# Kernel tuning notes

Hardware: AMD Instinct MI355X
Metric: run time of the kernel (lower is better)

Reference implementation:

```python
import jax, jax.numpy as jnp
import numpy as np
from jax import lax

B, C, H, W = 256, 7, 128, 128   # batch, num_bands, img_size, img_size
HID = 256                        # scorer hidden width
SEL = 3                          # selected_bands


def setup_inputs() -> dict:
    key = jax.random.key(0)
    k = jax.random.split(key, 7)
    n = H * W
    x = jax.random.normal(k[0], (B, C, H, W), dtype=jnp.float32)
    # to_qkv: Linear(num_bands, 3*num_bands); stored (in, out) for x @ w. Dead code
    # in the original forward (attn_output unused) but kept for parameter parity.
    w_qkv = jax.random.normal(k[1], (C, 3 * C), dtype=jnp.float32) * (1.0 / np.sqrt(C))
    b_qkv = jnp.zeros((3 * C,), dtype=jnp.float32)
    # band_score_proj: Linear(n, 256) -> ReLU -> Linear(256, 1)
    w1 = jax.random.normal(k[2], (n, HID), dtype=jnp.float32) * (1.0 / np.sqrt(n))
    b1 = jax.random.normal(k[3], (HID,), dtype=jnp.float32) * 0.01
    w2 = jax.random.normal(k[4], (HID, 1), dtype=jnp.float32) * (1.0 / np.sqrt(HID))
    b2 = jax.random.normal(k[5], (1,), dtype=jnp.float32) * 0.01
    return {"x": x, "w_qkv": w_qkv, "b_qkv": b_qkv, "w1": w1, "b1": b1, "w2": w2, "b2": b2}


def reference(x, w_qkv, b_qkv, w1, b1, w2, b2):
    b, c, h, w = x.shape
    feat = x.reshape(b, c, h * w)                  # b c n  (== x_flat.transpose(1,2))
    # NOTE: the original also runs a 1-dim-per-head SDPA on x_flat whose result
    # (attn_output) is never used in the returned values; it is omitted here.
    hid = jax.nn.relu(jnp.einsum('bcn,nk->bck', feat, w1) + b1)   # b c 256
    band_scores = (jnp.einsum('bck,ko->bco', hid, w2) + b2)[..., 0]  # b c
    _, top_indices = lax.top_k(band_scores, SEL)                  # b sel
    selected = jnp.take_along_axis(x, top_indices[:, :, None, None], axis=1)  # b sel h w
    return selected, top_indices
```

## Files before the change

### kernel.cpp

```cpp
#include <hip/hip_runtime.h>

#define Bn    256
#define Cc    7
#define Nn    16384
#define HIDW  256
#define SEL   3
#define Mrows (Bn * Cc)
#define KSPLIT 16
#define KCHUNK (Nn / KSPLIT)
#define BK    32
#define PART_STRIDE ((size_t)Mrows * HIDW)

typedef __attribute__((ext_vector_type(8))) short bf16x8;
typedef __attribute__((ext_vector_type(4))) float floatx4;

#if __has_builtin(__builtin_amdgcn_global_load_lds)
#define HAS_GLDS 1
#endif

#if __has_builtin(__builtin_amdgcn_sched_barrier)
#define SCHED_FENCE() __builtin_amdgcn_sched_barrier(0)
#else
#define SCHED_FENCE()
#endif

__device__ __forceinline__ unsigned pack_hi16(unsigned ua, unsigned ub) {
#if __has_builtin(__builtin_amdgcn_perm)
    return __builtin_amdgcn_perm(ub, ua, 0x07060302u);
#else
    return (ua >> 16) | (ub & 0xffff0000u);
#endif
}

__device__ __forceinline__ void split2(float a, float b, unsigned& hp, unsigned& lp) {
    unsigned ua = __float_as_uint(a), ub = __float_as_uint(b);
    float fa = __uint_as_float(ua & 0xffff0000u);
    float fb = __uint_as_float(ub & 0xffff0000u);
    float la = a - fa, lb = b - fb;
    hp = pack_hi16(ua, ub);
    lp = pack_hi16(__float_as_uint(la), __float_as_uint(lb));
}

__global__ __launch_bounds__(256) void convert_w1(const float* __restrict__ w1,
                                                  unsigned short* __restrict__ bhi,
                                                  unsigned short* __restrict__ blo) {
    const int id = blockIdx.x * 256 + threadIdx.x;
    const int l  = id & 63;
    const int ct = id >> 6;
    const int T  = ct & 15;
    const int c  = ct >> 4;
    const int n  = T * 16 + (l & 15);
    const int k  = c * 32 + (l >> 4) * 8;
    float f[8];
#pragma unroll
    for (int j = 0; j < 8; ++j) f[j] = w1[(size_t)(k + j) * HIDW + n];
    unsigned hp[4], lp[4];
#pragma unroll
    for (int m = 0; m < 4; ++m) split2(f[2 * m], f[2 * m + 1], hp[m], lp[m]);
    *(uint4*)(bhi + (size_t)id * 8) = make_uint4(hp[0], hp[1], hp[2], hp[3]);
    *(uint4*)(blo + (size_t)id * 8) = make_uint4(lp[0], lp[1], lp[2], lp[3]);
}

__global__ __launch_bounds__(256) void gemm_mfma(const float* __restrict__ A,
                                                 const unsigned short* __restrict__ Bhi,
                                                 const unsigned short* __restrict__ Blo,
                                                 float* __restrict__ part) {
    __shared__ unsigned short Ah[4096], Al[4096], Bh[4096], Bl[4096];

    const int bx = blockIdx.x;
    const int m0 = blockIdx.y * 128;
    const int s  = blockIdx.z;
    const int k0 = s * KCHUNK;
    const int t  = threadIdx.x;
    const int lane = t & 63;
    const int w    = t >> 6;
    const int wm   = w & 1;
    const int wn   = w >> 1;

    const int ar  = t >> 1;
    const int kof = (t & 1) * 16;
    const float* aptr = A + (size_t)(m0 + ar) * Nn + k0 + kof;
    const int aidx0 = (ar >> 4) * 512 + ((ar & 15) + ((kof >> 3) + 0) * 16) * 8;
    const int aidx1 = (ar >> 4) * 512 + ((ar & 15) + ((kof >> 3) + 1) * 16) * 8;
    const int wbase = (t & 192) * 8;

    floatx4 acc[4][4];
#pragma unroll
    for (int i = 0; i < 4; ++i)
#pragma unroll
        for (int j = 0; j < 4; ++j) acc[i][j] = (floatx4)0.0f;

    float4 pa0 = *(const float4*)(aptr + 0);
    float4 pa1 = *(const float4*)(aptr + 4);
    float4 pa2 = *(const float4*)(aptr + 8);
    float4 pa3 = *(const float4*)(aptr + 12);

    for (int kk = 0; kk < KCHUNK; kk += BK) {
        float af[16] = {pa0.x, pa0.y, pa0.z, pa0.w, pa1.x, pa1.y, pa1.z, pa1.w,
                        pa2.x, pa2.y, pa2.z, pa2.w, pa3.x, pa3.y, pa3.z, pa3.w};
        unsigned hp[8], lp[8];
#pragma unroll
        for (int m = 0; m < 8; ++m) split2(af[2 * m], af[2 * m + 1], hp[m], lp[m]);

        SCHED_FENCE();
        __builtin_amdgcn_s_barrier();
        SCHED_FENCE();

        const size_t bbase = ((size_t)(((k0 + kk) >> 5) * 16 + bx * 8)) * 512;
#ifdef HAS_GLDS
        __builtin_amdgcn_global_load_lds(
            (const __attribute__((address_space(1))) void*)(Bhi + bbase + t * 8),
            (__attribute__((address_space(3))) void*)&Bh[wbase], 16, 0, 0);
        __builtin_amdgcn_global_load_lds(
            (const __attribute__((address_space(1))) void*)(Bhi + bbase + 2048 + t * 8),
            (__attribute__((address_space(3))) void*)&Bh[2048 + wbase], 16, 0, 0);
        __builtin_amdgcn_global_load_lds(
            (const __attribute__((address_space(1))) void*)(Blo + bbase + t * 8),
            (__attribute__((address_space(3))) void*)&Bl[wbase], 16, 0, 0);
        __builtin_amdgcn_global_load_lds(
            (const __attribute__((address_space(1))) void*)(Blo + bbase + 2048 + t * 8),
            (__attribute__((address_space(3))) void*)&Bl[2048 + wbase], 16, 0, 0);
#else
        *(uint4*)&Bh[t * 8]        = *(const uint4*)(Bhi + bbase + t * 8);
        *(uint4*)&Bh[2048 + t * 8] = *(const uint4*)(Bhi + bbase + 2048 + t * 8);
        *(uint4*)&Bl[t * 8]        = *(const uint4*)(Blo + bbase + t * 8);
        *(uint4*)&Bl[2048 + t * 8] = *(const uint4*)(Blo + bbase + 2048 + t * 8);
#endif
        SCHED_FENCE();

        *(uint4*)&Ah[aidx0] = make_uint4(hp[0], hp[1], hp[2], hp[3]);
        *(uint4*)&Ah[aidx1] = make_uint4(hp[4], hp[5], hp[6], hp[7]);
        *(uint4*)&Al[aidx0] = make_uint4(lp[0], lp[1], lp[2], lp[3]);
        *(uint4*)&Al[aidx1] = make_uint4(lp[4], lp[5], lp[6], lp[7]);
        const int kn = (kk + BK < KCHUNK) ? (kk + BK) : kk;
        pa0 = *(const float4*)(aptr + kn + 0);
        pa1 = *(const float4*)(aptr + kn + 4);
        pa2 = *(const float4*)(aptr + kn + 8);
        pa3 = *(const float4*)(aptr + kn + 12);

        SCHED_FENCE();
#ifdef HAS_GLDS
        asm volatile("s_waitcnt vmcnt(4) lgkmcnt(0)" ::: "memory");
#else
        asm volatile("s_waitcnt vmcnt(4) lgkmcnt(0)" ::: "memory");
#endif
        __builtin_amdgcn_s_barrier();
        SCHED_FENCE();

        bf16x8 fah[4], fal[4], fbh[4], fbl[4];
#pragma unroll
        for (int i = 0; i < 4; ++i) {
            fah[i] = *(const bf16x8*)&Ah[(wm * 4 + i) * 512 + lane * 8];
            fal[i] = *(const bf16x8*)&Al[(wm * 4 + i) * 512 + lane * 8];
        }
#pragma unroll
        for (int j = 0; j < 4; ++j) {
            fbh[j] = *(const bf16x8*)&Bh[(wn * 4 + j) * 512 + lane * 8];
            fbl[j] = *(const bf16x8*)&Bl[(wn * 4 + j) * 512 + lane * 8];
        }
#pragma unroll
        for (int i = 0; i < 4; ++i)
#pragma unroll
            for (int j = 0; j < 4; ++j) {
                acc[i][j] = __builtin_amdgcn_mfma_f32_16x16x32_bf16(fah[i], fbh[j], acc[i][j], 0, 0, 0);
                acc[i][j] = __builtin_amdgcn_mfma_f32_16x16x32_bf16(fah[i], fbl[j], acc[i][j], 0, 0, 0);
                acc[i][j] = __builtin_amdgcn_mfma_f32_16x16x32_bf16(fal[i], fbh[j], acc[i][j], 0, 0, 0);
            }
    }

    const int row4 = (lane >> 4) * 4;
    const int col  = lane & 15;
    float* base = part + (size_t)s * PART_STRIDE;
#pragma unroll
    for (int i = 0; i < 4; ++i)
#pragma unroll
        for (int j = 0; j < 4; ++j) {
            const int n = bx * 128 + wn * 64 + j * 16 + col;
#pragma unroll
            for (int p = 0; p < 4; ++p) {
                const int m = m0 + wm * 64 + i * 16 + row4 + p;
                base[(size_t)m * HIDW + n] = acc[i][j][p];
            }
        }
}

__global__ __launch_bounds__(256) void score_rows(const float* __restrict__ part,
                                                  const float* __restrict__ b1,
                                                  const float* __restrict__ w2,
                                                  float* __restrict__ scores) {
    const int r = blockIdx.x;
    const int t = threadIdx.x;
    const size_t off = (size_t)r * HIDW + t;
    float h = 0.0f;
#pragma unroll
    for (int s = 0; s < KSPLIT; ++s) h += part[(size_t)s * PART_STRIDE + off];
    float p = fmaxf(h + b1[t], 0.0f) * w2[t];
#pragma unroll
    for (int o = 32; o > 0; o >>= 1) p += __shfl_down(p, o, 64);
    __shared__ float red[4];
    if ((t & 63) == 0) red[t >> 6] = p;
    __syncthreads();
    if (t == 0) scores[r] = red[0] + red[1] + red[2] + red[3];
}

__global__ __launch_bounds__(256) void gather_bands(const float* __restrict__ x,
                                                    const float* __restrict__ scores,
                                                    float* __restrict__ out) {
    const int id = blockIdx.x;
    const int b  = id / SEL;
    const int kk = id - b * SEL;
    float sc[Cc];
#pragma unroll
    for (int c = 0; c < Cc; ++c) sc[c] = scores[b * Cc + c];
    bool used[Cc] = {};
    int band = 0;
#pragma unroll
    for (int k = 0; k <= SEL - 1; ++k) {
        int best = 0;
        float bv = -3.4e38f;
#pragma unroll
        for (int c = 0; c < Cc; ++c)
            if (!used[c] && sc[c] > bv) { bv = sc[c]; best = c; }
        used[best] = true;
        if (k == kk) band = best;
        if (k > kk) break;
    }
    if (threadIdx.x == 0)
        out[(size_t)Bn * SEL * Nn + b * SEL + kk] = (float)band;
    const float4* src = (const float4*)(x + (size_t)(b * Cc + band) * Nn);
    float4* dst = (float4*)(out + (size_t)id * Nn);
    for (int i = threadIdx.x; i < Nn / 4; i += 256) dst[i] = src[i];
}

extern "C" void kernel_launch(void* const* d_in, const int* in_sizes, int n_in,
                              void* d_out, int out_size, void* d_ws, size_t ws_size,
                              hipStream_t stream) {
    const float* x  = (const float*)d_in[0];
    const float* w1 = (const float*)d_in[3];
    const float* b1 = (const float*)d_in[4];
    const float* w2 = (const float*)d_in[5];
    const float* b2 = (const float*)d_in[6];
    (void)b2;
    float* out = (float*)d_out;

    char* ws = (char*)d_ws;
    float* part = (float*)ws;
    unsigned short* bhi = (unsigned short*)(ws + KSPLIT * PART_STRIDE * sizeof(float));
    unsigned short* blo = bhi + (size_t)Nn * HIDW;
    float* scores = (float*)(blo + (size_t)Nn * HIDW);

    convert_w1<<<(Nn / 32) * 16 * 64 / 256, 256, 0, stream>>>(w1, bhi, blo);
    gemm_mfma<<<dim3(HIDW / 128, Mrows / 128, KSPLIT), 256, 0, stream>>>(x, bhi, blo, part);
    score_rows<<<Mrows, 256, 0, stream>>>(part, b1, w2, scores);
    gather_bands<<<Bn * SEL, 256, 0, stream>>>(x, scores, out);
}
```

Baseline: 256.3 us.

## Load MFMA fragments straight from global memory, drop LDS staging, remap block order

The GEMM kernel stops staging A and B tiles through shared memory with barriers. Each wave now loads its own A rows and pre-swizzled B fragments directly into registers and does the bf16 hi/lo split per fragment, so no LDS traffic or syncs remain. The grid becomes 1D with a custom mapping of block id to (n-tile, m-tile, k-split), probably chosen for L2 locality across the XCDs. The cost is redundant global loads: A is read twice per block (once per wn wave) and B twice (once per wm wave), which shifts pressure onto cache bandwidth.

New measurement: 295.6 us. 1.15x slower.

```diff
diff --git a/kernel.cpp b/kernel.cpp
--- a/kernel.cpp
+++ b/kernel.cpp
@@ -13,16 +13,7 @@
 
 typedef __attribute__((ext_vector_type(8))) short bf16x8;
 typedef __attribute__((ext_vector_type(4))) float floatx4;
-
-#if __has_builtin(__builtin_amdgcn_global_load_lds)
-#define HAS_GLDS 1
-#endif
-
-#if __has_builtin(__builtin_amdgcn_sched_barrier)
-#define SCHED_FENCE() __builtin_amdgcn_sched_barrier(0)
-#else
-#define SCHED_FENCE()
-#endif
+typedef __attribute__((ext_vector_type(4))) unsigned int uint32x4;
 
 __device__ __forceinline__ unsigned pack_hi16(unsigned ua, unsigned ub) {
 #if __has_builtin(__builtin_amdgcn_perm)
@@ -39,6 +30,22 @@
     float la = a - fa, lb = b - fb;
     hp = pack_hi16(ua, ub);
     lp = pack_hi16(__float_as_uint(la), __float_as_uint(lb));
+}
+
+__device__ __forceinline__ bf16x8 mk_bf16x8(unsigned a, unsigned b, unsigned c, unsigned d) {
+    uint32x4 u = {a, b, c, d};
+    return __builtin_bit_cast(bf16x8, u);
+}
+
+__device__ __forceinline__ void split_frag(const float4& x, const float4& y,
+                                           bf16x8& hi, bf16x8& lo) {
+    unsigned h0, h1, h2, h3, l0, l1, l2, l3;
+    split2(x.x, x.y, h0, l0);
+    split2(x.z, x.w, h1, l1);
+    split2(y.x, y.y, h2, l2);
+    split2(y.z, y.w, h3, l3);
+    hi = mk_bf16x8(h0, h1, h2, h3);
+    lo = mk_bf16x8(l0, l1, l2, l3);
 }
 
 __global__ __launch_bounds__(256) void convert_w1(const float* __restrict__ w1,
@@ -65,11 +72,15 @@
                                                  const unsigned short* __restrict__ Bhi,
                                                  const unsigned short* __restrict__ Blo,
                                                  float* __restrict__ part) {
-    __shared__ unsigned short Ah[4096], Al[4096], Bh[4096], Bl[4096];
-
-    const int bx = blockIdx.x;
-    const int m0 = blockIdx.y * 128;
-    const int s  = blockIdx.z;
+    const int id  = blockIdx.x;
+    const int r8  = id & 7;
+    const int bx  = (id >> 3) & 1;
+    const int q   = id >> 4;
+    const int ys  = r8 * 28 + q;
+    const int y   = ys % 14;
+    const int s   = ys / 14;
+
+    const int m0 = y * 128;
     const int k0 = s * KCHUNK;
     const int t  = threadIdx.x;
     const int lane = t & 63;
@@ -77,12 +88,10 @@
     const int wm   = w & 1;
     const int wn   = w >> 1;
 
-    const int ar  = t >> 1;
-    const int kof = (t & 1) * 16;
-    const float* aptr = A + (size_t)(m0 + ar) * Nn + k0 + kof;
-    const int aidx0 = (ar >> 4) * 512 + ((ar & 15) + ((kof >> 3) + 0) * 16) * 8;
-    const int aidx1 = (ar >> 4) * 512 + ((ar & 15) + ((kof >> 3) + 1) * 16) * 8;
-    const int wbase = (t & 192) * 8;
+    const float* aptr = A + (size_t)(m0 + wm * 64 + (lane & 15)) * Nn
+                          + k0 + (lane >> 4) * 8;
+    const unsigned short* bptr_h = Bhi + ((size_t)(k0 >> 5) * 16 + bx * 8 + wn * 4) * 512 + lane * 8;
+    const unsigned short* bptr_l = Blo + ((size_t)(k0 >> 5) * 16 + bx * 8 + wn * 4) * 512 + lane * 8;
 
     floatx4 acc[4][4];
 #pragma unroll
@@ -90,81 +99,39 @@
 #pragma unroll
         for (int j = 0; j < 4; ++j) acc[i][j] = (floatx4)0.0f;
 
-    float4 pa0 = *(const float4*)(aptr + 0);
-    float4 pa1 = *(const float4*)(aptr + 4);
-    float4 pa2 = *(const float4*)(aptr + 8);
-    float4 pa3 = *(const float4*)(aptr + 12);
-
+    float4 a[4][2];
+#pragma unroll
+    for (int i = 0; i < 4; ++i) {
+        a[i][0] = *(const float4*)(aptr + (size_t)i * 16 * Nn);
+        a[i][1] = *(const float4*)(aptr + (size_t)i * 16 * Nn + 4);
+    }
+
+#pragma unroll 2
     for (int kk = 0; kk < KCHUNK; kk += BK) {
-        float af[16] = {pa0.x, pa0.y, pa0.z, pa0.w, pa1.x, pa1.y, pa1.z, pa1.w,
-                        pa2.x, pa2.y, pa2.z, pa2.w, pa3.x, pa3.y, pa3.z, pa3.w};
-        unsigned hp[8], lp[8];
-#pragma unroll
-        for (int m = 0; m < 8; ++m) split2(af[2 * m], af[2 * m + 1], hp[m], lp[m]);
-
-        SCHED_FENCE();
-        __builtin_amdgcn_s_barrier();
-        SCHED_FENCE();
-
-        const size_t bbase = ((size_t)(((k0 + kk) >> 5) * 16 + bx * 8)) * 512;
-#ifdef HAS_GLDS
-        __builtin_amdgcn_global_load_lds(
-            (const __attribute__((address_space(1))) void*)(Bhi + bbase + t * 8),
-            (__attribute__((address_space(3))) void*)&Bh[wbase], 16, 0, 0);
-        __builtin_amdgcn_global_load_lds(
-            (const __attribute__((address_space(1))) void*)(Bhi + bbase + 2048 + t * 8),
-            (__attribute__((address_space(3))) void*)&Bh[2048 + wbase], 16, 0, 0);
-        __builtin_amdgcn_global_load_lds(
-            (const __attribute__((address_space(1))) void*)(Blo + bbase + t * 8),
-            (__attribute__((address_space(3))) void*)&Bl[wbase], 16, 0, 0);
-        __builtin_amdgcn_global_load_lds(
-            (const __attribute__((address_space(1))) void*)(Blo + bbase + 2048 + t * 8),
-            (__attribute__((address_space(3))) void*)&Bl[2048 + wbase], 16, 0, 0);
-#else
-        *(uint4*)&Bh[t * 8]        = *(const uint4*)(Bhi + bbase + t * 8);
-        *(uint4*)&Bh[2048 + t * 8] = *(const uint4*)(Bhi + bbase + 2048 + t * 8);
-        *(uint4*)&Bl[t * 8]        = *(const uint4*)(Blo + bbase + t * 8);
-        *(uint4*)&Bl[2048 + t * 8] = *(const uint4*)(Blo + bbase + 2048 + t * 8);
-#endif
-        SCHED_FENCE();
-
-        *(uint4*)&Ah[aidx0] = make_uint4(hp[0], hp[1], hp[2], hp[3]);
-        *(uint4*)&Ah[aidx1] = make_uint4(hp[4], hp[5], hp[6], hp[7]);
-        *(uint4*)&Al[aidx0] = make_uint4(lp[0], lp[1], lp[2], lp[3]);
-        *(uint4*)&Al[aidx1] = make_uint4(lp[4], lp[5], lp[6], lp[7]);
+        const unsigned short* bh = bptr_h + (size_t)(kk >> 5) * 8192;
+        const unsigned short* bl = bptr_l + (size_t)(kk >> 5) * 8192;
+        bf16x8 fbh[4], fbl[4];
+#pragma unroll
+        for (int j = 0; j < 4; ++j) {
+            fbh[j] = *(const bf16x8*)(bh + j * 512);
+            fbl[j] = *(const bf16x8*)(bl + j * 512);
+        }
+        bf16x8 ah[4], al[4];
+#pragma unroll
+        for (int i = 0; i < 4; ++i) split_frag(a[i][0], a[i][1], ah[i], al[i]);
         const int kn = (kk + BK < KCHUNK) ? (kk + BK) : kk;
-        pa0 = *(const float4*)(aptr + kn + 0);
-        pa1 = *(const float4*)(aptr + kn + 4);
-        pa2 = *(const float4*)(aptr + kn + 8);
-        pa3 = *(const float4*)(aptr + kn + 12);
-
-        SCHED_FENCE();
-#ifdef HAS_GLDS
-        asm volatile("s_waitcnt vmcnt(4) lgkmcnt(0)" ::: "memory");
-#else
-        asm volatile("s_waitcnt vmcnt(4) lgkmcnt(0)" ::: "memory");
-#endif
-        __builtin_amdgcn_s_barrier();
-        SCHED_FENCE();
-
-        bf16x8 fah[4], fal[4], fbh[4], fbl[4];
 #pragma unroll
         for (int i = 0; i < 4; ++i) {
-            fah[i] = *(const bf16x8*)&Ah[(wm * 4 + i) * 512 + lane * 8];
-            fal[i] = *(const bf16x8*)&Al[(wm * 4 + i) * 512 + lane * 8];
+            a[i][0] = *(const float4*)(aptr + (size_t)i * 16 * Nn + kn);
+            a[i][1] = *(const float4*)(aptr + (size_t)i * 16 * Nn + kn + 4);
         }
 #pragma unroll
-        for (int j = 0; j < 4; ++j) {
-            fbh[j] = *(const bf16x8*)&Bh[(wn * 4 + j) * 512 + lane * 8];
-            fbl[j] = *(const bf16x8*)&Bl[(wn * 4 + j) * 512 + lane * 8];
-        }
-#pragma unroll
         for (int i = 0; i < 4; ++i)
 #pragma unroll
             for (int j = 0; j < 4; ++j) {
-                acc[i][j] = __builtin_amdgcn_mfma_f32_16x16x32_bf16(fah[i], fbh[j], acc[i][j], 0, 0, 0);
-                acc[i][j] = __builtin_amdgcn_mfma_f32_16x16x32_bf16(fah[i], fbl[j], acc[i][j], 0, 0, 0);
-                acc[i][j] = __builtin_amdgcn_mfma_f32_16x16x32_bf16(fal[i], fbh[j], acc[i][j], 0, 0, 0);
+                acc[i][j] = __builtin_amdgcn_mfma_f32_16x16x32_bf16(ah[i], fbh[j], acc[i][j], 0, 0, 0);
+                acc[i][j] = __builtin_amdgcn_mfma_f32_16x16x32_bf16(ah[i], fbl[j], acc[i][j], 0, 0, 0);
+                acc[i][j] = __builtin_amdgcn_mfma_f32_16x16x32_bf16(al[i], fbh[j], acc[i][j], 0, 0, 0);
             }
     }
 
@@ -250,7 +217,7 @@
     float* scores = (float*)(blo + (size_t)Nn * HIDW);
 
     convert_w1<<<(Nn / 32) * 16 * 64 / 256, 256, 0, stream>>>(w1, bhi, blo);
-    gemm_mfma<<<dim3(HIDW / 128, Mrows / 128, KSPLIT), 256, 0, stream>>>(x, bhi, blo, part);
+    gemm_mfma<<<14 * 2 * KSPLIT, 256, 0, stream>>>(x, bhi, blo, part);
     score_rows<<<Mrows, 256, 0, stream>>>(part, b1, w2, scores);
     gather_bands<<<Bn * SEL, 256, 0, stream>>>(x, scores, out);
 }
```
